# Kernel tuning notes

Hardware: AMD Instinct MI355X
Metric: run time of the kernel (lower is better)

## Reference

```python
import jax, jax.numpy as jnp
import numpy as np

N_NODES = 100_000
N_EDGES = 1_600_000
IN_DIM, HIDDEN, Z_DIM = 64, 128, 64


def _gcn_conv(x, src, dst, dinv, W, b, n):
    # PyG GCNConv: out_i = sum_j (d_i^-1/2 d_j^-1/2) (x_j @ W) + b, edges incl. self-loops
    xw = x @ W                                   # [N, out]
    norm = dinv[src] * dinv[dst]                 # [E+N]
    msg = xw[src] * norm[:, None]                # [E+N, out]
    return jax.ops.segment_sum(msg, dst, num_segments=n) + b


def _prep_graph(edge_index, n):
    loop = jnp.arange(n, dtype=edge_index.dtype)
    src = jnp.concatenate([edge_index[0], loop])
    dst = jnp.concatenate([edge_index[1], loop])
    deg = jax.ops.segment_sum(jnp.ones_like(dst, dtype=jnp.float32), dst, num_segments=n)
    dinv = jnp.where(deg > 0, jax.lax.rsqrt(jnp.maximum(deg, 1.0)), 0.0)
    return src, dst, dinv


def setup_inputs() -> dict:
    key = jax.random.key(0)
    ks = jax.random.split(key, 8)
    x = jax.random.normal(ks[0], (N_NODES, IN_DIM), dtype=jnp.float32)
    edge_index = jax.random.randint(ks[1], (2, N_EDGES), 0, N_NODES, dtype=jnp.int32)

    def glorot(k, fi, fo):
        s = (6.0 / (fi + fo)) ** 0.5
        return jax.random.uniform(k, (fi, fo), jnp.float32, -s, s)

    return {
        "x": x, "edge_index": edge_index,
        "W1": glorot(ks[2], IN_DIM, HIDDEN), "b1": jnp.zeros((HIDDEN,), jnp.float32),
        "W2": glorot(ks[3], HIDDEN, HIDDEN), "b2": jnp.zeros((HIDDEN,), jnp.float32),
        "Wmu": glorot(ks[4], HIDDEN, Z_DIM), "bmu": jnp.zeros((Z_DIM,), jnp.float32),
        "Wlv": glorot(ks[5], HIDDEN, Z_DIM), "blv": jnp.zeros((Z_DIM,), jnp.float32),
    }


def reference(x, edge_index, W1, b1, W2, b2, Wmu, bmu, Wlv, blv):
    n = x.shape[0]
    src, dst, dinv = _prep_graph(edge_index, n)
    h = jax.nn.relu(_gcn_conv(x, src, dst, dinv, W1, b1, n))
    h = jax.nn.relu(_gcn_conv(h, src, dst, dinv, W2, b2, n))
    # dropout p=0.0 (eval): identity
    mu = _gcn_conv(h, src, dst, dinv, Wmu, bmu, n)
    logvar = _gcn_conv(h, src, dst, dinv, Wlv, blv, n)
    return (mu, logvar)
```

## Files before the change

kernel.cpp:

```cpp
#include <hip/hip_runtime.h>
#include <hip/hip_fp16.h>
#include <cstddef>

#define N_NODES 100000
#define N_EDGES 1600000
#define E_TOT   (N_EDGES + N_NODES)
#define IN_DIM  64
#define HIDDEN  128
#define Z_DIM   64

#define BN 128
#define NB ((N_NODES + BN - 1) / BN)
#define NBLK 256

using f16x8 = __attribute__((ext_vector_type(8))) _Float16;
using f32x4 = __attribute__((ext_vector_type(4))) float;


__global__ __launch_bounds__(256) void count_k(const int* __restrict__ dst, int* cnt, int e) {
    int i = blockIdx.x * 256 + threadIdx.x;
    if (i < e) atomicAdd(&cnt[dst[i]], 1);
}

__global__ __launch_bounds__(256) void scan_block_k(const int* __restrict__ cnt, int* __restrict__ rowptr,
                                                    int* __restrict__ bsum, float* __restrict__ dinv, int n) {
    __shared__ int s[256];
    int tid = threadIdx.x;
    int i = blockIdx.x * 256 + tid;
    int v = (i < n) ? cnt[i] + 1 : 0;
    if (i < n) dinv[i] = rsqrtf((float)v);
    s[tid] = v;
    __syncthreads();
#pragma unroll
    for (int off = 1; off < 256; off <<= 1) {
        int t = (tid >= off) ? s[tid - off] : 0;
        __syncthreads();
        s[tid] += t;
        __syncthreads();
    }
    if (i < n) rowptr[i] = s[tid] - v;
    if (tid == 255) bsum[blockIdx.x] = s[255];
}

__global__ __launch_bounds__(512) void scan_bsum_k(int* bsum, int nb) {
    __shared__ int s[512];
    int tid = threadIdx.x;
    int v = (tid < nb) ? bsum[tid] : 0;
    s[tid] = v;
    __syncthreads();
#pragma unroll
    for (int off = 1; off < 512; off <<= 1) {
        int t = (tid >= off) ? s[tid - off] : 0;
        __syncthreads();
        s[tid] += t;
        __syncthreads();
    }
    if (tid < nb) bsum[tid] = s[tid] - v;
}

__global__ __launch_bounds__(256) void scan_add_k(int* __restrict__ rowptr, const int* __restrict__ bsum,
                                                  int* __restrict__ ebase, int* __restrict__ bcur,
                                                  int n, int etot, int e) {
    int i = blockIdx.x * 256 + threadIdx.x;
    if (i < n) {
        int val = rowptr[i] + bsum[blockIdx.x];
        rowptr[i] = val;
        if ((i & (BN - 1)) == 0) {
            int b = i >> 7;
            int eb = val - b * BN;
            ebase[b] = eb;
            bcur[b] = eb;
        }
    }
    if (i == 0) { rowptr[n] = etot; ebase[NB] = e; }
}

__global__ __launch_bounds__(256) void binA_k(const int* __restrict__ src, const int* __restrict__ dst,
                                              int* __restrict__ bcur, int* __restrict__ binned, int e) {
    __shared__ int hist[NB];
    __shared__ int cur[NB];
    int t = threadIdx.x;
    int ch = (e + gridDim.x - 1) / gridDim.x;
    int i0 = blockIdx.x * ch;
    int i1 = i0 + ch; if (i1 > e) i1 = e;

    for (int b = t; b < NB; b += 256) hist[b] = 0;
    __syncthreads();
    for (int i = i0 + t; i < i1; i += 256)
        atomicAdd(&hist[dst[i] >> 7], 1);
    __syncthreads();
    for (int b = t; b < NB; b += 256) {
        int h = hist[b];
        cur[b] = h ? atomicAdd(&bcur[b], h) : 0;
    }
    __syncthreads();
    for (int i = i0 + t; i < i1; i += 256) {
        int s = src[i], d = dst[i];
        int p = atomicAdd(&cur[d >> 7], 1);
        binned[p] = ((d & 127) << 17) | s;
    }
}

__global__ __launch_bounds__(256) void place_k(const int* __restrict__ binned, const int* __restrict__ ebase,
                                               const int* __restrict__ rowptr, const float* __restrict__ dinv,
                                               int2* __restrict__ em, int n) {
    __shared__ int cur[BN];
    __shared__ float sdv[BN];
    int b = blockIdx.x, t = threadIdx.x;
    int n0 = b * BN;
    int nn = n - n0; if (nn > BN) nn = BN;
    if (t < nn) {
        int rp = rowptr[n0 + t];
        float dv = dinv[n0 + t];
        sdv[t] = dv;
        em[rp] = make_int2(n0 + t, __float_as_int(dv * dv));
        cur[t] = rp + 1;
    }
    __syncthreads();
    int e0 = ebase[b], e1 = ebase[b + 1];
    for (int i = e0 + t; i < e1; i += 256) {
        int pk = binned[i];
        int ld = pk >> 17, s = pk & 0x1FFFF;
        int q = atomicAdd(&cur[ld], 1);
        em[q] = make_int2(s, __float_as_int(dinv[s] * sdv[ld]));
    }
}

__global__ __launch_bounds__(256) void cast16_k(const float* __restrict__ in, __half* __restrict__ out, int total8) {
    int i = blockIdx.x * 256 + threadIdx.x;
    if (i >= total8) return;
    const float4* in4 = (const float4*)in;
    float4 a = in4[2 * i], b = in4[2 * i + 1];
    __half2 h0 = __floats2half2_rn(a.x, a.y);
    __half2 h1 = __floats2half2_rn(a.z, a.w);
    __half2 h2 = __floats2half2_rn(b.x, b.y);
    __half2 h3 = __floats2half2_rn(b.z, b.w);
    uint4 pk = make_uint4(*(unsigned*)&h0, *(unsigned*)&h1, *(unsigned*)&h2, *(unsigned*)&h3);
    ((uint4*)out)[i] = pk;
}

__global__ __launch_bounds__(256) void wprep_k(const float* __restrict__ W1, const float* __restrict__ W2,
                                               const float* __restrict__ Wmu, const float* __restrict__ Wlv,
                                               __half* __restrict__ W1t, __half* __restrict__ W2t,
                                               __half* __restrict__ Wht) {
    int i = blockIdx.x * 256 + threadIdx.x;
    if (i < 128 * 64) {
        int col = i >> 6, k = i & 63;
        W1t[i] = __float2half(W1[k * 128 + col]);
    }
    int j = i - 128 * 64;
    if (j >= 0 && j < 128 * 128) {
        int col = j >> 7, k = j & 127;
        W2t[j] = __float2half(W2[k * 128 + col]);
    }
    int m = i - 128 * 64 - 128 * 128;
    if (m >= 0 && m < 128 * 128) {
        int col = m >> 7, k = m & 127;
        Wht[m] = __float2half(col < 64 ? Wmu[k * 64 + col] : Wlv[k * 64 + (col - 64)]);
    }
}


template <int DIM, bool HEAD>
__global__ __launch_bounds__(256) void agg_k(const __half* __restrict__ H, const int* __restrict__ rowptr,
                                             const int2* __restrict__ em, __half* __restrict__ out,
                                             const float* __restrict__ bmu, const float* __restrict__ blv,
                                             float* __restrict__ mu, float* __restrict__ lv, int n) {
    int node = (int)((blockIdx.x * 256 + threadIdx.x) >> 6);
    if (node >= n) return;
    int lane = threadIdx.x & 63;
    int beg = rowptr[node], end = rowptr[node + 1];
    const uint4* H4 = (const uint4*)H;

    constexpr int RV   = DIM / 8;
    constexpr int SUBS = 64 / RV;
    constexpr int STEP = SUBS * 2;
    int sub = lane / RV;
    int fl  = lane % RV;

    float acc[8];
#pragma unroll
    for (int q = 0; q < 8; q++) acc[q] = 0.f;

    auto meta = [&](int j, int p, int& s, float& w) {
        int idx = j + SUBS * p + sub;
        int ci  = idx < end ? idx : beg;
        int2 e  = em[ci];
        s = e.x;
        w = idx < end ? __int_as_float(e.y) : 0.f;
    };
    auto rows = [&](int s0, int s1, uint4& r0, uint4& r1) {
        r0 = H4[(size_t)s0 * RV + fl];
        r1 = H4[(size_t)s1 * RV + fl];
    };
    auto fmas = [&](const uint4& r0, const uint4& r1, float ww0, float ww1) {
        const __half* h0 = (const __half*)&r0;
        const __half* h1 = (const __half*)&r1;
#pragma unroll
        for (int q = 0; q < 8; q++) acc[q] = fmaf(ww0, __half2float(h0[q]), acc[q]);
#pragma unroll
        for (int q = 0; q < 8; q++) acc[q] = fmaf(ww1, __half2float(h1[q]), acc[q]);
    };

    int G = (end - beg + STEP - 1) / STEP;

    int   sa0, sa1, sb0, sb1, sc0, sc1, sd0, sd1;
    float wa0, wa1, wb0, wb1, wc0, wc1, wd0, wd1;
    uint4 ra0, ra1, rb0, rb1, rc0, rc1, rd0, rd1;

    meta(beg,            0, sa0, wa0); meta(beg,            1, sa1, wa1);
    meta(beg + STEP,     0, sb0, wb0); meta(beg + STEP,     1, sb1, wb1);
    rows(sa0, sa1, ra0, ra1);
    rows(sb0, sb1, rb0, rb1);
    meta(beg + 2 * STEP, 0, sc0, wc0); meta(beg + 2 * STEP, 1, sc1, wc1);
    meta(beg + 3 * STEP, 0, sd0, wd0); meta(beg + 3 * STEP, 1, sd1, wd1);

    int g = 0;
    int jf = beg + 4 * STEP;
    while (true) {
        rows(sc0, sc1, rc0, rc1);
        fmas(ra0, ra1, wa0, wa1);
        if (++g >= G) break;
        meta(jf, 0, sa0, wa0); meta(jf, 1, sa1, wa1); jf += STEP;

        rows(sd0, sd1, rd0, rd1);
        fmas(rb0, rb1, wb0, wb1);
        if (++g >= G) break;
        meta(jf, 0, sb0, wb0); meta(jf, 1, sb1, wb1); jf += STEP;

        rows(sa0, sa1, ra0, ra1);
        fmas(rc0, rc1, wc0, wc1);
        if (++g >= G) break;
        meta(jf, 0, sc0, wc0); meta(jf, 1, sc1, wc1); jf += STEP;

        rows(sb0, sb1, rb0, rb1);
        fmas(rd0, rd1, wd0, wd1);
        if (++g >= G) break;
        meta(jf, 0, sd0, wd0); meta(jf, 1, sd1, wd1); jf += STEP;
    }

#pragma unroll
    for (int off = 32; off >= RV; off >>= 1) {
#pragma unroll
        for (int q = 0; q < 8; q++) acc[q] += __shfl_xor(acc[q], off);
    }
    if (sub == 0) {
        if constexpr (HEAD) {
            const float* bp = (fl < 8) ? (bmu + fl * 8) : (blv + (fl - 8) * 8);
#pragma unroll
            for (int q = 0; q < 8; q++) acc[q] += bp[q];
            float* op = (fl < 8) ? (mu + (size_t)node * 64 + fl * 8)
                                 : (lv + (size_t)node * 64 + (fl - 8) * 8);
            *(float4*)op = make_float4(acc[0], acc[1], acc[2], acc[3]);
            *(float4*)(op + 4) = make_float4(acc[4], acc[5], acc[6], acc[7]);
        } else {
            __half2 q0 = __floats2half2_rn(acc[0], acc[1]);
            __half2 q1 = __floats2half2_rn(acc[2], acc[3]);
            __half2 q2 = __floats2half2_rn(acc[4], acc[5]);
            __half2 q3 = __floats2half2_rn(acc[6], acc[7]);
            uint4 pk = make_uint4(*(unsigned*)&q0, *(unsigned*)&q1, *(unsigned*)&q2, *(unsigned*)&q3);
            *(uint4*)(out + (size_t)node * DIM + fl * 8) = pk;
        }
    }
}


template <int K, bool BR>
__global__ __launch_bounds__(256) void mgemm_k(const __half* __restrict__ A,
                                               const __half* __restrict__ Wt,
                                               const float* __restrict__ bias,
                                               __half* __restrict__ C, int n) {
    __shared__ __align__(16) __half Wl[128 * K];
    int t = threadIdx.x;

    constexpr int CHUNKS = 128 * K / 8;
    const uint4* Wg = (const uint4*)Wt;
    for (int i = t; i < CHUNKS; i += 256) {
        int g = i * 16;
        int col = g / (2 * K);
        uint4 v = Wg[i];
        *(uint4*)((char*)Wl + (g ^ ((col & 7) << 4))) = v;
    }
    __syncthreads();

    int lane = t & 63, w = t >> 6;
    int colb = lane & 15;
    int kq = (lane >> 4) * 8;
    int m0 = blockIdx.x * 64 + w * 16;
    int rowA = m0 + colb; if (rowA >= n) rowA = n - 1;
    const __half* Arow = A + (size_t)rowA * K + kq;

    f32x4 acc[8];
#pragma unroll
    for (int c = 0; c < 8; c++) acc[c] = (f32x4){0.f, 0.f, 0.f, 0.f};

    const char* wb = (const char*)Wl;
    int swz = (colb & 7) << 4;
    int off0 = colb * (2 * K) + kq * 2;

#pragma unroll
    for (int k0 = 0; k0 < K; k0 += 32) {
        f16x8 a = *(const f16x8*)(Arow + k0);
#pragma unroll
        for (int c = 0; c < 8; c++) {
            f16x8 b = *(const f16x8*)(wb + ((off0 + c * (32 * K) + k0 * 2) ^ swz));
            acc[c] = __builtin_amdgcn_mfma_f32_16x16x32_f16(a, b, acc[c], 0, 0, 0);
        }
    }

    int rbase = m0 + (lane >> 4) * 4;
#pragma unroll
    for (int c = 0; c < 8; c++) {
        int col = c * 16 + colb;
        float bv = BR ? bias[col] : 0.f;
#pragma unroll
        for (int r = 0; r < 4; r++) {
            int row = rbase + r;
            if (row < n) {
                float v = acc[c][r] + bv;
                if (BR) v = fmaxf(v, 0.f);
                C[(size_t)row * 128 + col] = __float2half(v);
            }
        }
    }
}


extern "C" void kernel_launch(void* const* d_in, const int* in_sizes, int n_in,
                              void* d_out, int out_size, void* d_ws, size_t ws_size,
                              hipStream_t stream) {
    const int N = N_NODES, E = N_EDGES, ETOT = E_TOT;

    const float* x    = (const float*)d_in[0];
    const int*   ei   = (const int*)d_in[1];
    const int*   srcA = ei;
    const int*   dstA = ei + E;
    const float* W1   = (const float*)d_in[2];
    const float* b1   = (const float*)d_in[3];
    const float* W2   = (const float*)d_in[4];
    const float* b2   = (const float*)d_in[5];
    const float* Wmu  = (const float*)d_in[6];
    const float* bmu  = (const float*)d_in[7];
    const float* Wlv  = (const float*)d_in[8];
    const float* blv  = (const float*)d_in[9];
    float* out = (float*)d_out;

    char* ws = (char*)d_ws;
    size_t o = 0;
    auto alloc = [&](size_t bytes) -> void* {
        o = (o + 255) & ~(size_t)255;
        void* p = ws + o;
        o += bytes;
        return p;
    };
    int*    cnt    = (int*)alloc((size_t)N * 4);
    int*    rowptr = (int*)alloc((size_t)(N + 1) * 4);
    float*  dinv   = (float*)alloc((size_t)N * 4);
    int*    bsum   = (int*)alloc(512 * 4);
    int*    ebase  = (int*)alloc((size_t)(NB + 1) * 4);
    int*    bcur   = (int*)alloc((size_t)(NB + 1) * 4);
    int2*   em     = (int2*)alloc((size_t)ETOT * 8);
    int*    binned = (int*)alloc((size_t)E * 4);
    __half* x16    = (__half*)alloc((size_t)N * IN_DIM * 2);
    __half* B1     = (__half*)alloc((size_t)N * HIDDEN * 2);
    __half* B2     = (__half*)alloc((size_t)N * HIDDEN * 2);
    __half* W1t    = (__half*)alloc(128 * 64 * 2);
    __half* W2t    = (__half*)alloc(128 * 128 * 2);
    __half* Wht    = (__half*)alloc(128 * 128 * 2);
    (void)ws_size;

    const int gN = (N + 255) / 256;
    const int gE = (E + 255) / 256;
    const int gAgg = (N + 3) / 4;
    const int gMg  = (N + 63) / 64;
    const int gCast = (N * IN_DIM / 8 + 255) / 256;

    hipMemsetAsync(cnt, 0, (size_t)N * 4, stream);
    count_k<<<gE, 256, 0, stream>>>(dstA, cnt, E);
    scan_block_k<<<gN, 256, 0, stream>>>(cnt, rowptr, bsum, dinv, N);
    scan_bsum_k<<<1, 512, 0, stream>>>(bsum, gN);
    scan_add_k<<<gN, 256, 0, stream>>>(rowptr, bsum, ebase, bcur, N, ETOT, E);
    binA_k<<<NBLK, 256, 0, stream>>>(srcA, dstA, bcur, binned, E);
    place_k<<<NB, 256, 0, stream>>>(binned, ebase, rowptr, dinv, em, N);
    wprep_k<<<160, 256, 0, stream>>>(W1, W2, Wmu, Wlv, W1t, W2t, Wht);
    cast16_k<<<gCast, 256, 0, stream>>>(x, x16, N * IN_DIM / 8);

    agg_k<64, false><<<gAgg, 256, 0, stream>>>(x16, rowptr, em, B1, nullptr, nullptr, nullptr, nullptr, N);
    mgemm_k<64, true><<<gMg, 256, 0, stream>>>(B1, W1t, b1, B2, N);

    agg_k<128, false><<<gAgg, 256, 0, stream>>>(B2, rowptr, em, B1, nullptr, nullptr, nullptr, nullptr, N);
    mgemm_k<128, true><<<gMg, 256, 0, stream>>>(B1, W2t, b2, B2, N);

    mgemm_k<128, false><<<gMg, 256, 0, stream>>>(B2, Wht, nullptr, B1, N);
    agg_k<128, true><<<gAgg, 256, 0, stream>>>(B1, rowptr, em, nullptr, bmu, blv,
                                               out, out + (size_t)N * Z_DIM, N);
}
```

Before: 430.7 us.

## Pad CSR rows to multiples of 16 and fuse preprocessing kernels

Each node's edge list is padded to a multiple of 16 with zero-weight dummy entries, so the aggregation loop can drop per-edge bounds checks and use an exact group count. The padding needs a second scan to keep raw edge offsets for the binning step, and the memset, weight cast and x cast are folded into one prep kernel. The block-sum scan and scan-add are merged, and the degree count reads dst as int4. The cost is extra memory traffic and wasted FMAs on the padded entries, plus a loop in place_k that writes the padding.

```diff
diff --git a/kernel.cpp b/kernel.cpp
--- a/kernel.cpp
+++ b/kernel.cpp
@@ -12,67 +12,127 @@
 #define BN 128
 #define NB ((N_NODES + BN - 1) / BN)
 #define NBLK 256
+#define GN  ((N_NODES + 255) / 256)
+
+#define EM_CAP (E_TOT + 15 * N_NODES + 64)
 
 using f16x8 = __attribute__((ext_vector_type(8))) _Float16;
 using f32x4 = __attribute__((ext_vector_type(4))) float;
 
 
-__global__ __launch_bounds__(256) void count_k(const int* __restrict__ dst, int* cnt, int e) {
+__global__ __launch_bounds__(256) void prep_k(const float* __restrict__ x, __half* __restrict__ x16,
+                                              const float* __restrict__ W1, const float* __restrict__ W2,
+                                              const float* __restrict__ Wmu, const float* __restrict__ Wlv,
+                                              __half* __restrict__ W1t, __half* __restrict__ W2t,
+                                              __half* __restrict__ Wht, int* __restrict__ cnt) {
     int i = blockIdx.x * 256 + threadIdx.x;
-    if (i < e) atomicAdd(&cnt[dst[i]], 1);
+    const int CAST = N_NODES * IN_DIM / 8;
+    if (i < CAST) {
+        const float4* in4 = (const float4*)x;
+        float4 a = in4[2 * i], b = in4[2 * i + 1];
+        __half2 h0 = __floats2half2_rn(a.x, a.y);
+        __half2 h1 = __floats2half2_rn(a.z, a.w);
+        __half2 h2 = __floats2half2_rn(b.x, b.y);
+        __half2 h3 = __floats2half2_rn(b.z, b.w);
+        uint4 pk = make_uint4(*(unsigned*)&h0, *(unsigned*)&h1, *(unsigned*)&h2, *(unsigned*)&h3);
+        ((uint4*)x16)[i] = pk;
+        return;
+    }
+    int j = i - CAST;
+    if (j < 128 * 64) {
+        int col = j >> 6, k = j & 63;
+        W1t[j] = __float2half(W1[k * 128 + col]);
+        return;
+    }
+    int m = j - 128 * 64;
+    if (m < 128 * 128) {
+        int col = m >> 7, k = m & 127;
+        W2t[m] = __float2half(W2[k * 128 + col]);
+        return;
+    }
+    int h = m - 128 * 128;
+    if (h < 128 * 128) {
+        int col = h >> 7, k = h & 127;
+        Wht[h] = __float2half(col < 64 ? Wmu[k * 64 + col] : Wlv[k * 64 + (col - 64)]);
+        return;
+    }
+    int z = h - 128 * 128;
+    if (z < N_NODES / 4) ((int4*)cnt)[z] = make_int4(0, 0, 0, 0);
+}
+
+
+__global__ __launch_bounds__(256) void count4_k(const int* __restrict__ dst, int* cnt, int e4) {
+    int i = blockIdx.x * 256 + threadIdx.x;
+    if (i < e4) {
+        int4 d = ((const int4*)dst)[i];
+        atomicAdd(&cnt[d.x], 1);
+        atomicAdd(&cnt[d.y], 1);
+        atomicAdd(&cnt[d.z], 1);
+        atomicAdd(&cnt[d.w], 1);
+    }
 }
 
 __global__ __launch_bounds__(256) void scan_block_k(const int* __restrict__ cnt, int* __restrict__ rowptr,
-                                                    int* __restrict__ bsum, float* __restrict__ dinv, int n) {
-    __shared__ int s[256];
+                                                    int2* __restrict__ bsum, int* __restrict__ rawAt,
+                                                    float* __restrict__ dinv, int n) {
+    __shared__ int sp[256], sr[256];
     int tid = threadIdx.x;
     int i = blockIdx.x * 256 + tid;
-    int v = (i < n) ? cnt[i] + 1 : 0;
-    if (i < n) dinv[i] = rsqrtf((float)v);
-    s[tid] = v;
+    int deg = (i < n) ? cnt[i] + 1 : 0;
+    int pad = (deg + 15) & ~15;
+    int raw = (i < n) ? deg - 1 : 0;
+    if (i < n) dinv[i] = rsqrtf((float)deg);
+    sp[tid] = pad; sr[tid] = raw;
     __syncthreads();
 #pragma unroll
     for (int off = 1; off < 256; off <<= 1) {
-        int t = (tid >= off) ? s[tid - off] : 0;
+        int t1 = (tid >= off) ? sp[tid - off] : 0;
+        int t2 = (tid >= off) ? sr[tid - off] : 0;
         __syncthreads();
-        s[tid] += t;
+        sp[tid] += t1; sr[tid] += t2;
         __syncthreads();
     }
-    if (i < n) rowptr[i] = s[tid] - v;
-    if (tid == 255) bsum[blockIdx.x] = s[255];
-}
-
-__global__ __launch_bounds__(512) void scan_bsum_k(int* bsum, int nb) {
-    __shared__ int s[512];
+    if (i < n) rowptr[i] = sp[tid] - pad;
+    if (i < n && tid == 0)   rawAt[i >> 7] = 0;
+    if (i < n && tid == 128) rawAt[i >> 7] = sr[127];
+    if (tid == 255) bsum[blockIdx.x] = make_int2(sp[255], sr[255]);
+}
+
+__global__ __launch_bounds__(512) void scan_addm_k(int* __restrict__ rowptr, const int2* __restrict__ bsum,
+                                                   const int* __restrict__ rawAt, int* __restrict__ ebase,
+                                                   int* __restrict__ bcur, int n, int e, int nb) {
+    __shared__ int sp[512], sr[512];
+    __shared__ int tot;
     int tid = threadIdx.x;
-    int v = (tid < nb) ? bsum[tid] : 0;
-    s[tid] = v;
+    int2 v = (tid < nb) ? bsum[tid] : make_int2(0, 0);
+    sp[tid] = v.x; sr[tid] = v.y;
     __syncthreads();
 #pragma unroll
     for (int off = 1; off < 512; off <<= 1) {
-        int t = (tid >= off) ? s[tid - off] : 0;
+        int t1 = (tid >= off) ? sp[tid - off] : 0;
+        int t2 = (tid >= off) ? sr[tid - off] : 0;
         __syncthreads();
-        s[tid] += t;
+        sp[tid] += t1; sr[tid] += t2;
         __syncthreads();
     }
-    if (tid < nb) bsum[tid] = s[tid] - v;
-}
-
-__global__ __launch_bounds__(256) void scan_add_k(int* __restrict__ rowptr, const int* __restrict__ bsum,
-                                                  int* __restrict__ ebase, int* __restrict__ bcur,
-                                                  int n, int etot, int e) {
-    int i = blockIdx.x * 256 + threadIdx.x;
-    if (i < n) {
-        int val = rowptr[i] + bsum[blockIdx.x];
-        rowptr[i] = val;
-        if ((i & (BN - 1)) == 0) {
-            int b = i >> 7;
-            int eb = val - b * BN;
-            ebase[b] = eb;
-            bcur[b] = eb;
+    if (tid == 511) tot = sp[511];
+    __syncthreads();
+    sp[tid] -= v.x; sr[tid] -= v.y;
+    __syncthreads();
+    if (tid < 256) {
+        int i = blockIdx.x * 256 + tid;
+        if (i < n) {
+            int val = rowptr[i] + sp[blockIdx.x];
+            rowptr[i] = val;
+            if ((i & 127) == 0) {
+                int b = i >> 7;
+                int eb = rawAt[b] + sr[b >> 1];
+                ebase[b] = eb;
+                bcur[b] = eb;
+            }
         }
-    }
-    if (i == 0) { rowptr[n] = etot; ebase[NB] = e; }
+        if (i == 0) { rowptr[n] = tot; ebase[NB] = e; }
+    }
 }
 
 __global__ __launch_bounds__(256) void binA_k(const int* __restrict__ src, const int* __restrict__ dst,
@@ -124,39 +184,11 @@
         int q = atomicAdd(&cur[ld], 1);
         em[q] = make_int2(s, __float_as_int(dinv[s] * sdv[ld]));
     }
-}
-
-__global__ __launch_bounds__(256) void cast16_k(const float* __restrict__ in, __half* __restrict__ out, int total8) {
-    int i = blockIdx.x * 256 + threadIdx.x;
-    if (i >= total8) return;
-    const float4* in4 = (const float4*)in;
-    float4 a = in4[2 * i], b = in4[2 * i + 1];
-    __half2 h0 = __floats2half2_rn(a.x, a.y);
-    __half2 h1 = __floats2half2_rn(a.z, a.w);
-    __half2 h2 = __floats2half2_rn(b.x, b.y);
-    __half2 h3 = __floats2half2_rn(b.z, b.w);
-    uint4 pk = make_uint4(*(unsigned*)&h0, *(unsigned*)&h1, *(unsigned*)&h2, *(unsigned*)&h3);
-    ((uint4*)out)[i] = pk;
-}
-
-__global__ __launch_bounds__(256) void wprep_k(const float* __restrict__ W1, const float* __restrict__ W2,
-                                               const float* __restrict__ Wmu, const float* __restrict__ Wlv,
-                                               __half* __restrict__ W1t, __half* __restrict__ W2t,
-                                               __half* __restrict__ Wht) {
-    int i = blockIdx.x * 256 + threadIdx.x;
-    if (i < 128 * 64) {
-        int col = i >> 6, k = i & 63;
-        W1t[i] = __float2half(W1[k * 128 + col]);
-    }
-    int j = i - 128 * 64;
-    if (j >= 0 && j < 128 * 128) {
-        int col = j >> 7, k = j & 127;
-        W2t[j] = __float2half(W2[k * 128 + col]);
-    }
-    int m = i - 128 * 64 - 128 * 128;
-    if (m >= 0 && m < 128 * 128) {
-        int col = m >> 7, k = m & 127;
-        Wht[m] = __float2half(col < 64 ? Wmu[k * 64 + col] : Wlv[k * 64 + (col - 64)]);
+    __syncthreads();
+    if (t < nn) {
+        int pe = rowptr[n0 + t + 1];
+        int node = n0 + t;
+        for (int p = cur[t]; p < pe; p++) em[p] = make_int2(node, 0);
     }
 }
 
@@ -170,6 +202,7 @@
     if (node >= n) return;
     int lane = threadIdx.x & 63;
     int beg = rowptr[node], end = rowptr[node + 1];
+    int lastIdx = rowptr[n] - 1;
     const uint4* H4 = (const uint4*)H;
 
     constexpr int RV   = DIM / 8;
@@ -183,11 +216,11 @@
     for (int q = 0; q < 8; q++) acc[q] = 0.f;
 
     auto meta = [&](int j, int p, int& s, float& w) {
-        int idx = j + SUBS * p + sub;
-        int ci  = idx < end ? idx : beg;
-        int2 e  = em[ci];
+        int ci = j + SUBS * p + sub;
+        ci = min(ci, lastIdx);
+        int2 e = em[ci];
         s = e.x;
-        w = idx < end ? __int_as_float(e.y) : 0.f;
+        w = __int_as_float(e.y);
     };
     auto rows = [&](int s0, int s1, uint4& r0, uint4& r1) {
         r0 = H4[(size_t)s0 * RV + fl];
@@ -202,7 +235,7 @@
         for (int q = 0; q < 8; q++) acc[q] = fmaf(ww1, __half2float(h1[q]), acc[q]);
     };
 
-    int G = (end - beg + STEP - 1) / STEP;
+    int G = (end - beg) / STEP;
 
     int   sa0, sa1, sb0, sb1, sc0, sc1, sd0, sd1;
     float wa0, wa1, wb0, wb1, wc0, wc1, wd0, wd1;
@@ -329,7 +362,7 @@
 extern "C" void kernel_launch(void* const* d_in, const int* in_sizes, int n_in,
                               void* d_out, int out_size, void* d_ws, size_t ws_size,
                               hipStream_t stream) {
-    const int N = N_NODES, E = N_EDGES, ETOT = E_TOT;
+    const int N = N_NODES, E = N_EDGES;
 
     const float* x    = (const float*)d_in[0];
     const int*   ei   = (const int*)d_in[1];
@@ -356,10 +389,11 @@
     int*    cnt    = (int*)alloc((size_t)N * 4);
     int*    rowptr = (int*)alloc((size_t)(N + 1) * 4);
     float*  dinv   = (float*)alloc((size_t)N * 4);
-    int*    bsum   = (int*)alloc(512 * 4);
+    int2*   bsum   = (int2*)alloc(512 * 8);
+    int*    rawAt  = (int*)alloc((size_t)NB * 4);
     int*    ebase  = (int*)alloc((size_t)(NB + 1) * 4);
     int*    bcur   = (int*)alloc((size_t)(NB + 1) * 4);
-    int2*   em     = (int2*)alloc((size_t)ETOT * 8);
+    int2*   em     = (int2*)alloc((size_t)EM_CAP * 8);
     int*    binned = (int*)alloc((size_t)E * 4);
     __half* x16    = (__half*)alloc((size_t)N * IN_DIM * 2);
     __half* B1     = (__half*)alloc((size_t)N * HIDDEN * 2);
@@ -369,21 +403,18 @@
     __half* Wht    = (__half*)alloc(128 * 128 * 2);
     (void)ws_size;
 
-    const int gN = (N + 255) / 256;
-    const int gE = (E + 255) / 256;
+    const int PREP_T = N * IN_DIM / 8 + 128 * 64 + 128 * 128 + 128 * 128 + N / 4;
+    const int gPrep = (PREP_T + 255) / 256;
+    const int gC4  = (E / 4 + 255) / 256;
     const int gAgg = (N + 3) / 4;
     const int gMg  = (N + 63) / 64;
-    const int gCast = (N * IN_DIM / 8 + 255) / 256;
-
-    hipMemsetAsync(cnt, 0, (size_t)N * 4, stream);
-    count_k<<<gE, 256, 0, stream>>>(dstA, cnt, E);
-    scan_block_k<<<gN, 256, 0, stream>>>(cnt, rowptr, bsum, dinv, N);
-    scan_bsum_k<<<1, 512, 0, stream>>>(bsum, gN);
-    scan_add_k<<<gN, 256, 0, stream>>>(rowptr, bsum, ebase, bcur, N, ETOT, E);
+
+    prep_k<<<gPrep, 256, 0, stream>>>(x, x16, W1, W2, Wmu, Wlv, W1t, W2t, Wht, cnt);
+    count4_k<<<gC4, 256, 0, stream>>>(dstA, cnt, E / 4);
+    scan_block_k<<<GN, 256, 0, stream>>>(cnt, rowptr, bsum, rawAt, dinv, N);
+    scan_addm_k<<<GN, 512, 0, stream>>>(rowptr, bsum, rawAt, ebase, bcur, N, E, GN);
     binA_k<<<NBLK, 256, 0, stream>>>(srcA, dstA, bcur, binned, E);
     place_k<<<NB, 256, 0, stream>>>(binned, ebase, rowptr, dinv, em, N);
-    wprep_k<<<160, 256, 0, stream>>>(W1, W2, Wmu, Wlv, W1t, W2t, Wht);
-    cast16_k<<<gCast, 256, 0, stream>>>(x, x16, N * IN_DIM / 8);
 
     agg_k<64, false><<<gAgg, 256, 0, stream>>>(x16, rowptr, em, B1, nullptr, nullptr, nullptr, nullptr, N);
     mgemm_k<64, true><<<gMg, 256, 0, stream>>>(B1, W1t, b1, B2, N);
```

Result: no change. 425.7 us (-1.2%).
